# Kernel tuning notes

Measured on AMD Instinct MI355X. Metric: run time of the kernel, lower is better.

Reference implementation:

```python
import jax, jax.numpy as jnp
import numpy as np

N, E, IN, HID, OUT, H, G = 50000, 800000, 128, 32, 32, 4, 64
NEG_SLOPE = 0.2


def setup_inputs() -> dict:
    key = jax.random.key(0)
    ks = jax.random.split(key, 12)
    p = lambda k, s: jax.random.normal(k, s, jnp.float32) * 0.1
    x = jax.random.normal(ks[0], (N, IN), jnp.float32)
    edge_index = jax.random.randint(ks[1], (2, E), 0, N, dtype=jnp.int64)
    batch = jnp.sort(jax.random.randint(ks[2], (N,), 0, G, dtype=jnp.int64))
    return {
        'x': x, 'edge_index': edge_index, 'batch': batch,
        'W1': p(ks[3], (IN, H * HID)),
        'att_src1': p(ks[4], (H, HID)), 'att_dst1': p(ks[5], (H, HID)),
        'b1': jnp.zeros((H * HID,), jnp.float32),
        'W2': p(ks[6], (H * HID, H * OUT)),
        'att_src2': p(ks[7], (H, OUT)), 'att_dst2': p(ks[8], (H, OUT)),
        'b2': jnp.zeros((H * OUT,), jnp.float32),
        'lin_w': p(ks[9], (H * OUT, 1)),
        'lin_b': jnp.zeros((1,), jnp.float32),
    }


def gat_conv(x, src, dst, W, a_src, a_dst, b, heads, ch):
    # x: [N, F_in]; src/dst: [E'] with self-loops already appended.
    n = x.shape[0]
    h = (x @ W).reshape(n, heads, ch)                      # [N, H, C]
    alpha_s = jnp.einsum('nhc,hc->nh', h, a_src)           # [N, H]
    alpha_d = jnp.einsum('nhc,hc->nh', h, a_dst)
    e = jax.nn.leaky_relu(alpha_s[src] + alpha_d[dst], NEG_SLOPE)  # [E', H]
    # segment softmax over destination neighborhoods
    m = jax.ops.segment_max(e, dst, num_segments=n)
    m = jnp.where(jnp.isfinite(m), m, 0.0)
    ex = jnp.exp(e - m[dst])
    s = jax.ops.segment_sum(ex, dst, num_segments=n)
    alpha = ex / (s[dst] + 1e-16)                          # [E', H]
    out = jax.ops.segment_sum(alpha[:, :, None] * h[src], dst, num_segments=n)
    return out.reshape(n, heads * ch) + b


def reference(x, edge_index, batch, W1, att_src1, att_dst1, b1,
              W2, att_src2, att_dst2, b2, lin_w, lin_b):
    # add self-loops (PyG GATConv default add_self_loops=True)
    loops = jnp.arange(N, dtype=edge_index.dtype)
    src = jnp.concatenate([edge_index[0], loops])
    dst = jnp.concatenate([edge_index[1], loops])

    h = jax.nn.elu(gat_conv(x, src, dst, W1, att_src1, att_dst1, b1, H, HID))
    h = gat_conv(h, src, dst, W2, att_src2, att_dst2, b2, H, OUT)  # [N, H*OUT]

    # global mean + max pool per graph
    counts = jax.ops.segment_sum(jnp.ones((N,), h.dtype), batch, num_segments=G)
    mean_p = jax.ops.segment_sum(h, batch, num_segments=G) / jnp.maximum(counts, 1.0)[:, None]
    max_p = jax.ops.segment_max(h, batch, num_segments=G)
    max_p = jnp.where(jnp.isfinite(max_p), max_p, 0.0)
    pooled = mean_p + max_p                                # [G, H*OUT]
    return pooled @ lin_w + lin_b                          # [G, 1]
```

## Files before the change

### kernel.cpp

```cpp
#include <hip/hip_runtime.h>
#include <hip/hip_bf16.h>
#include <hip/hip_fp16.h>
#include <math.h>

#define NEG_SLOPE 0.2f
#define BCAP 80
#define LAYER_W 16384

typedef _Float16 half8 __attribute__((ext_vector_type(8)));
typedef _Float16 half4v __attribute__((ext_vector_type(4)));
typedef float f32x4 __attribute__((ext_vector_type(4)));


__device__ __forceinline__ int lbound(const int* __restrict__ a, int n, int key) {
    int lo = 0, hi = n;
    while (lo < hi) {
        int mid = (lo + hi) >> 1;
        if (a[mid] < key) lo = mid + 1; else hi = mid;
    }
    return lo;
}

__device__ __forceinline__ unsigned encf(float f) {
    unsigned u = __float_as_uint(f);
    return (u & 0x80000000u) ? ~u : (u | 0x80000000u);
}
__device__ __forceinline__ float decf(unsigned u) {
    return (u & 0x80000000u) ? __uint_as_float(u & 0x7FFFFFFFu) : __uint_as_float(~u);
}


__global__ void init_kernel(int* __restrict__ cnt, int* __restrict__ col,
                            float* __restrict__ gsum, unsigned* __restrict__ gmax,
                            int n, int gtot) {
    int i = blockIdx.x * blockDim.x + threadIdx.x;
    if (i < n) {
        cnt[i] = 1;
        col[(size_t)i * BCAP] = i;
    }
    if (i < gtot) { gsum[i] = 0.f; gmax[i] = 0x007FFFFFu;  }
}

__global__ void build_kernel(const int* __restrict__ src, const int* __restrict__ dst,
                             int* __restrict__ cnt, int* __restrict__ col, int E) {
    int i = blockIdx.x * blockDim.x + threadIdx.x;
    if (i >= E) return;
    int d = dst[i];
    int slot = atomicAdd(&cnt[d], 1);
    if (slot < BCAP) col[(size_t)d * BCAP + slot] = src[i];
}


__global__ void wprep_kernel(const float* __restrict__ W1, const float* __restrict__ W2,
                             _Float16* __restrict__ wt_hi, _Float16* __restrict__ wt_lo) {
    int b = blockIdx.x;
    int layer = b >> 5;
    int nt = (b >> 2) & 7;
    int kc = b & 3;
    const float* W = layer ? W2 : W1;
    int lane = threadIdx.x;
    int n = lane & 15, q = lane >> 4;
    size_t base = (size_t)layer * LAYER_W + (size_t)((nt * 4 + kc) * 64 + lane) * 8;
    #pragma unroll
    for (int j = 0; j < 8; ++j) {
        int k = kc * 32 + q * 8 + j;
        float w = W[(size_t)k * 128 + nt * 16 + n];
        _Float16 hi = (_Float16)w;
        wt_hi[base + j] = hi;
        wt_lo[base + j] = (_Float16)(w - (float)hi);
    }
}


__global__ __launch_bounds__(256) void gemm_attn_kernel(
        const float* __restrict__ A,
        const _Float16* __restrict__ wt_hi, const _Float16* __restrict__ wt_lo,
        const float* __restrict__ att_src, const float* __restrict__ att_dst,
        _Float16* __restrict__ H16, float* __restrict__ as_, float* __restrict__ ad_,
        int M) {
    __shared__ _Float16 a_hi[64][136];
    __shared__ _Float16 a_lo[64][136];

    int tid = threadIdx.x;
    int m0 = blockIdx.x * 64;

    #pragma unroll
    for (int t = 0; t < 8; ++t) {
        int f = tid + t * 256;
        int r = f >> 5;
        int c4 = (f & 31) << 2;
        int gr = m0 + r; if (gr >= M) gr = M - 1;
        const float4 v = *(const float4*)(A + (size_t)gr * 128 + c4);
        _Float16 h0 = (_Float16)v.x, h1 = (_Float16)v.y;
        _Float16 h2 = (_Float16)v.z, h3 = (_Float16)v.w;
        half4v hi = { h0, h1, h2, h3 };
        half4v lo = { (_Float16)(v.x - (float)h0), (_Float16)(v.y - (float)h1),
                      (_Float16)(v.z - (float)h2), (_Float16)(v.w - (float)h3) };
        *(half4v*)&a_hi[r][c4] = hi;
        *(half4v*)&a_lo[r][c4] = lo;
    }
    __syncthreads();

    int w = tid >> 6;
    int lane = tid & 63;
    int cbase = lane & 15;
    int q = lane >> 4;
    int mrow = (w << 4) + cbase;

    f32x4 acc[8];
    #pragma unroll
    for (int nt = 0; nt < 8; ++nt) acc[nt] = (f32x4){0.f, 0.f, 0.f, 0.f};

    #pragma unroll
    for (int kc = 0; kc < 4; ++kc) {
        half8 ah = *(half8*)&a_hi[mrow][kc * 32 + q * 8];
        half8 al = *(half8*)&a_lo[mrow][kc * 32 + q * 8];
        #pragma unroll
        for (int nt = 0; nt < 8; ++nt) {
            const half8 bh = *(const half8*)(wt_hi + (size_t)((nt * 4 + kc) * 64 + lane) * 8);
            const half8 bl = *(const half8*)(wt_lo + (size_t)((nt * 4 + kc) * 64 + lane) * 8);
            acc[nt] = __builtin_amdgcn_mfma_f32_16x16x32_f16(ah, bh, acc[nt], 0, 0, 0);
            acc[nt] = __builtin_amdgcn_mfma_f32_16x16x32_f16(al, bh, acc[nt], 0, 0, 0);
            acc[nt] = __builtin_amdgcn_mfma_f32_16x16x32_f16(ah, bl, acc[nt], 0, 0, 0);
        }
    }

    float ps[4][4], pd[4][4];
    #pragma unroll
    for (int h = 0; h < 4; ++h)
        #pragma unroll
        for (int i = 0; i < 4; ++i) { ps[h][i] = 0.f; pd[h][i] = 0.f; }

    #pragma unroll
    for (int nt = 0; nt < 8; ++nt) {
        int c = nt * 16 + cbase;
        float sv = att_src[c], dv = att_dst[c];
        int h = nt >> 1;
        #pragma unroll
        for (int i = 0; i < 4; ++i) {
            ps[h][i] += acc[nt][i] * sv;
            pd[h][i] += acc[nt][i] * dv;
            int gr = m0 + (w << 4) + (q << 2) + i;
            if (gr < M) H16[(size_t)gr * 128 + c] = (_Float16)acc[nt][i];
        }
    }
    #pragma unroll
    for (int h = 0; h < 4; ++h)
        #pragma unroll
        for (int i = 0; i < 4; ++i) {
            float a = ps[h][i], b = pd[h][i];
            #pragma unroll
            for (int off = 1; off < 16; off <<= 1) {
                a += __shfl_xor(a, off, 64);
                b += __shfl_xor(b, off, 64);
            }
            if (cbase == 0) {
                int gr = m0 + (w << 4) + (q << 2) + i;
                if (gr < M) { as_[(size_t)gr * 4 + h] = a; ad_[(size_t)gr * 4 + h] = b; }
            }
        }
}


__global__ __launch_bounds__(256) void agg_kernel(
        const int* __restrict__ cnt, const int* __restrict__ col,
        const _Float16* __restrict__ h16, const float* __restrict__ as_,
        const float* __restrict__ ad_, const float* __restrict__ bias,
        float* __restrict__ out, int n, int elu) {
    __shared__ int   s_col[4][64];
    __shared__ float s_w[4][256];
    __shared__ int   s_nchunk;

    int wvb  = threadIdx.x >> 6;
    int lane = threadIdx.x & 63;
    int wv   = blockIdx.x * 4 + wvb;
    int valid = (wv < n);
    if (!valid) wv = n - 1;

    int deg = cnt[wv]; if (deg > BCAP) deg = BCAP;
    const int* crow = col + (size_t)wv * BCAP;
    const float4 adv = *(const float4*)(ad_ + (size_t)wv * 4);

    if (threadIdx.x == 0) s_nchunk = 0;
    __syncthreads();
    if (lane == 0) atomicMax(&s_nchunk, (deg + 63) >> 6);
    __syncthreads();
    int nchunk = s_nchunk;

    int q = lane >> 4;
    int r = lane & 15;
    int head = r >> 2;
    const _Float16* hrow = h16 + 8 * r;

    float l0 = 0.f, l1 = 0.f, l2 = 0.f, l3 = 0.f;
    float acc[8];
    #pragma unroll
    for (int j = 0; j < 8; ++j) acc[j] = 0.f;

    for (int c = 0; c < nchunk; ++c) {
        int c0 = c << 6;
        int cl = deg - c0;
        cl = cl < 0 ? 0 : (cl > 64 ? 64 : cl);
        if (lane < cl) {
            int s = crow[c0 + lane];
            const float4 av = *(const float4*)(as_ + (size_t)s * 4);
            float e0 = av.x + adv.x, e1 = av.y + adv.y;
            float e2 = av.z + adv.z, e3 = av.w + adv.w;
            float w0 = __expf(fmaxf(e0, NEG_SLOPE * e0));
            float w1 = __expf(fmaxf(e1, NEG_SLOPE * e1));
            float w2 = __expf(fmaxf(e2, NEG_SLOPE * e2));
            float w3 = __expf(fmaxf(e3, NEG_SLOPE * e3));
            l0 += w0; l1 += w1; l2 += w2; l3 += w3;
            s_col[wvb][lane] = s;
            *(float4*)&s_w[wvb][lane * 4] = make_float4(w0, w1, w2, w3);
        } else {
            s_col[wvb][lane] = 0;
            *(float4*)&s_w[wvb][lane * 4] = make_float4(0.f, 0.f, 0.f, 0.f);
        }
        __syncthreads();
        for (int it = 0; it < cl; it += 16) {
            int ea = it + q;
            int eb = ea + 4;
            int ec = ea + 8;
            int ed = ea + 12;
            int sa = s_col[wvb][ea];
            int sb = s_col[wvb][eb];
            int sc = s_col[wvb][ec];
            int sd = s_col[wvb][ed];
            float wa = s_w[wvb][ea * 4 + head];
            float wb = s_w[wvb][eb * 4 + head];
            float wc = s_w[wvb][ec * 4 + head];
            float wd = s_w[wvb][ed * 4 + head];
            const half8 ha = *(const half8*)(hrow + (size_t)sa * 128);
            const half8 hb = *(const half8*)(hrow + (size_t)sb * 128);
            const half8 hc = *(const half8*)(hrow + (size_t)sc * 128);
            const half8 hd = *(const half8*)(hrow + (size_t)sd * 128);
            #pragma unroll
            for (int j = 0; j < 8; ++j)
                acc[j] += wa * (float)ha[j] + wb * (float)hb[j]
                        + wc * (float)hc[j] + wd * (float)hd[j];
        }
        __syncthreads();
    }

    #pragma unroll
    for (int j = 0; j < 8; ++j) {
        acc[j] += __shfl_xor(acc[j], 16, 64);
        acc[j] += __shfl_xor(acc[j], 32, 64);
    }

    #pragma unroll
    for (int off = 1; off < 64; off <<= 1) {
        l0 += __shfl_xor(l0, off, 64);
        l1 += __shfl_xor(l1, off, 64);
        l2 += __shfl_xor(l2, off, 64);
        l3 += __shfl_xor(l3, off, 64);
    }

    if (lane < 16 && valid) {
        float lh = head == 0 ? l0 : head == 1 ? l1 : head == 2 ? l2 : l3;
        float inv = 1.f / (lh + 1e-16f);
        const float4 bv0 = *(const float4*)(bias + 8 * r);
        const float4 bv1 = *(const float4*)(bias + 8 * r + 4);
        float o[8];
        o[0] = acc[0] * inv + bv0.x; o[1] = acc[1] * inv + bv0.y;
        o[2] = acc[2] * inv + bv0.z; o[3] = acc[3] * inv + bv0.w;
        o[4] = acc[4] * inv + bv1.x; o[5] = acc[5] * inv + bv1.y;
        o[6] = acc[6] * inv + bv1.z; o[7] = acc[7] * inv + bv1.w;
        if (elu) {
            #pragma unroll
            for (int j = 0; j < 8; ++j) o[j] = o[j] > 0.f ? o[j] : expm1f(o[j]);
        }
        *(float4*)(out + (size_t)wv * 128 + 8 * r)     = make_float4(o[0], o[1], o[2], o[3]);
        *(float4*)(out + (size_t)wv * 128 + 8 * r + 4) = make_float4(o[4], o[5], o[6], o[7]);
    }
}


__global__ void pool1_kernel(const float* __restrict__ h, const int* __restrict__ batch,
                             float* __restrict__ gsum, unsigned* __restrict__ gmax, int n) {
    int g = blockIdx.x >> 3;
    int p = blockIdx.x & 7;
    int c = threadIdx.x;
    int s = lbound(batch, n, g);
    int e = lbound(batch, n, g + 1);
    int len = e - s;
    int lo = s + (int)((long long)len * p / 8);
    int hi = s + (int)((long long)len * (p + 1) / 8);
    float sum = 0.f, mx = -INFINITY;
    for (int i = lo; i < hi; ++i) {
        float v = h[(size_t)i * 128 + c];
        sum += v; mx = fmaxf(mx, v);
    }
    if (hi > lo) {
        atomicAdd(&gsum[g * 128 + c], sum);
        atomicMax(&gmax[g * 128 + c], encf(mx));
    }
}

__global__ void pool2_kernel(const float* __restrict__ gsum, const unsigned* __restrict__ gmax,
                             const int* __restrict__ batch, const float* __restrict__ lin_w,
                             const float* __restrict__ lin_b, float* __restrict__ out, int n) {
    int g = blockIdx.x;
    int c = threadIdx.x;
    int s = lbound(batch, n, g);
    int e = lbound(batch, n, g + 1);
    float cnt = fmaxf((float)(e - s), 1.0f);
    float mean = gsum[g * 128 + c] / cnt;
    float mx = decf(gmax[g * 128 + c]);
    if (!isfinite(mx)) mx = 0.f;
    float v = (mean + mx) * lin_w[c];
    __shared__ float red[128];
    red[c] = v;
    __syncthreads();
    for (int off = 64; off > 0; off >>= 1) {
        if (c < off) red[c] += red[c + off];
        __syncthreads();
    }
    if (c == 0) out[g] = red[0] + lin_b[0];
}


extern "C" void kernel_launch(void* const* d_in, const int* in_sizes, int n_in,
                              void* d_out, int out_size, void* d_ws, size_t ws_size,
                              hipStream_t stream) {
    const float* x    = (const float*)d_in[0];
    const int*   ei   = (const int*)d_in[1];
    const int*   batch= (const int*)d_in[2];
    const float* W1   = (const float*)d_in[3];
    const float* at_s1= (const float*)d_in[4];
    const float* at_d1= (const float*)d_in[5];
    const float* b1   = (const float*)d_in[6];
    const float* W2   = (const float*)d_in[7];
    const float* at_s2= (const float*)d_in[8];
    const float* at_d2= (const float*)d_in[9];
    const float* b2   = (const float*)d_in[10];
    const float* lw   = (const float*)d_in[11];
    const float* lb   = (const float*)d_in[12];
    float* out = (float*)d_out;

    const int N = in_sizes[0] / 128;
    const int E = in_sizes[1] / 2;
    const int G = out_size;

    char* p = (char*)d_ws;
    auto carve = [&](size_t bytes) -> void* {
        void* q = (void*)p;
        p += (bytes + 255) & ~(size_t)255;
        return q;
    };
    _Float16* h16    = (_Float16*)carve((size_t)N * 128 * 2);
    float*    agg    = (float*)carve((size_t)N * 128 * 4);
    float*    asb    = (float*)carve((size_t)N * 4 * 4);
    float*    adb    = (float*)carve((size_t)N * 4 * 4);
    int*      cnt    = (int*)carve((size_t)N * 4);
    int*      col    = (int*)carve((size_t)N * BCAP * 4);
    float*    gsum   = (float*)carve((size_t)G * 128 * 4);
    unsigned* gmax   = (unsigned*)carve((size_t)G * 128 * 4);
    _Float16* wt_hi  = (_Float16*)carve((size_t)2 * LAYER_W * 2);
    _Float16* wt_lo  = (_Float16*)carve((size_t)2 * LAYER_W * 2);

    const int* esrc = ei;
    const int* edst = ei + E;

    int initN = (N > G * 128) ? N : G * 128;
    init_kernel<<<(initN + 255) / 256, 256, 0, stream>>>(cnt, col, gsum, gmax, N, G * 128);
    build_kernel<<<(E + 255) / 256, 256, 0, stream>>>(esrc, edst, cnt, col, E);
    wprep_kernel<<<64, 64, 0, stream>>>(W1, W2, wt_hi, wt_lo);

    gemm_attn_kernel<<<(N + 63) / 64, 256, 0, stream>>>(
        x, wt_hi, wt_lo, at_s1, at_d1, h16, asb, adb, N);
    agg_kernel<<<(N + 3) / 4, 256, 0, stream>>>(cnt, col, h16, asb, adb, b1, agg, N, 1);

    gemm_attn_kernel<<<(N + 63) / 64, 256, 0, stream>>>(
        agg, wt_hi + LAYER_W, wt_lo + LAYER_W, at_s2, at_d2, h16, asb, adb, N);
    agg_kernel<<<(N + 3) / 4, 256, 0, stream>>>(cnt, col, h16, asb, adb, b2, agg, N, 0);

    pool1_kernel<<<G * 8, 128, 0, stream>>>(agg, batch, gsum, gmax, N);
    pool2_kernel<<<G, 128, 0, stream>>>(gsum, gmax, batch, lw, lb, out, N);
}
```

Before: 311.9 us.

## Fold attention vectors into weights as extra GEMM tile; sum softmax denominators during aggregation

```diff
diff --git a/kernel.cpp b/kernel.cpp
--- a/kernel.cpp
+++ b/kernel.cpp
@@ -5,7 +5,7 @@
 
 #define NEG_SLOPE 0.2f
 #define BCAP 80
-#define LAYER_W 16384
+#define LAYER_W 18432
 
 typedef _Float16 half8 __attribute__((ext_vector_type(8)));
 typedef _Float16 half4v __attribute__((ext_vector_type(4)));
@@ -52,19 +52,32 @@
 
 
 __global__ void wprep_kernel(const float* __restrict__ W1, const float* __restrict__ W2,
+                             const float* __restrict__ as1, const float* __restrict__ ad1,
+                             const float* __restrict__ as2, const float* __restrict__ ad2,
                              _Float16* __restrict__ wt_hi, _Float16* __restrict__ wt_lo) {
     int b = blockIdx.x;
-    int layer = b >> 5;
-    int nt = (b >> 2) & 7;
-    int kc = b & 3;
-    const float* W = layer ? W2 : W1;
+    int layer = b / 36;
+    int rem = b % 36;
+    int nt = rem >> 2;
+    int kc = rem & 3;
+    const float* W  = layer ? W2 : W1;
+    const float* As = layer ? as2 : as1;
+    const float* Ad = layer ? ad2 : ad1;
     int lane = threadIdx.x;
     int n = lane & 15, q = lane >> 4;
     size_t base = (size_t)layer * LAYER_W + (size_t)((nt * 4 + kc) * 64 + lane) * 8;
     #pragma unroll
     for (int j = 0; j < 8; ++j) {
         int k = kc * 32 + q * 8 + j;
-        float w = W[(size_t)k * 128 + nt * 16 + n];
+        float w = 0.f;
+        if (nt < 8) {
+            w = W[(size_t)k * 128 + nt * 16 + n];
+        } else if (n < 4) {
+            for (int c = 0; c < 32; ++c) w += W[(size_t)k * 128 + n * 32 + c] * As[n * 32 + c];
+        } else if (n < 8) {
+            int hh = n - 4;
+            for (int c = 0; c < 32; ++c) w += W[(size_t)k * 128 + hh * 32 + c] * Ad[hh * 32 + c];
+        }
         _Float16 hi = (_Float16)w;
         wt_hi[base + j] = hi;
         wt_lo[base + j] = (_Float16)(w - (float)hi);
@@ -75,7 +88,6 @@
 __global__ __launch_bounds__(256) void gemm_attn_kernel(
         const float* __restrict__ A,
         const _Float16* __restrict__ wt_hi, const _Float16* __restrict__ wt_lo,
-        const float* __restrict__ att_src, const float* __restrict__ att_dst,
         _Float16* __restrict__ H16, float* __restrict__ as_, float* __restrict__ ad_,
         int M) {
     __shared__ _Float16 a_hi[64][136];
@@ -107,16 +119,16 @@
     int q = lane >> 4;
     int mrow = (w << 4) + cbase;
 
-    f32x4 acc[8];
-    #pragma unroll
-    for (int nt = 0; nt < 8; ++nt) acc[nt] = (f32x4){0.f, 0.f, 0.f, 0.f};
+    f32x4 acc[9];
+    #pragma unroll
+    for (int nt = 0; nt < 9; ++nt) acc[nt] = (f32x4){0.f, 0.f, 0.f, 0.f};
 
     #pragma unroll
     for (int kc = 0; kc < 4; ++kc) {
         half8 ah = *(half8*)&a_hi[mrow][kc * 32 + q * 8];
         half8 al = *(half8*)&a_lo[mrow][kc * 32 + q * 8];
         #pragma unroll
-        for (int nt = 0; nt < 8; ++nt) {
+        for (int nt = 0; nt < 9; ++nt) {
             const half8 bh = *(const half8*)(wt_hi + (size_t)((nt * 4 + kc) * 64 + lane) * 8);
             const half8 bl = *(const half8*)(wt_lo + (size_t)((nt * 4 + kc) * 64 + lane) * 8);
             acc[nt] = __builtin_amdgcn_mfma_f32_16x16x32_f16(ah, bh, acc[nt], 0, 0, 0);
@@ -125,40 +137,25 @@
         }
     }
 
-    float ps[4][4], pd[4][4];
-    #pragma unroll
-    for (int h = 0; h < 4; ++h)
-        #pragma unroll
-        for (int i = 0; i < 4; ++i) { ps[h][i] = 0.f; pd[h][i] = 0.f; }
-
     #pragma unroll
     for (int nt = 0; nt < 8; ++nt) {
         int c = nt * 16 + cbase;
-        float sv = att_src[c], dv = att_dst[c];
-        int h = nt >> 1;
         #pragma unroll
         for (int i = 0; i < 4; ++i) {
-            ps[h][i] += acc[nt][i] * sv;
-            pd[h][i] += acc[nt][i] * dv;
             int gr = m0 + (w << 4) + (q << 2) + i;
             if (gr < M) H16[(size_t)gr * 128 + c] = (_Float16)acc[nt][i];
         }
     }
-    #pragma unroll
-    for (int h = 0; h < 4; ++h)
+    if (cbase < 8) {
         #pragma unroll
         for (int i = 0; i < 4; ++i) {
-            float a = ps[h][i], b = pd[h][i];
-            #pragma unroll
-            for (int off = 1; off < 16; off <<= 1) {
-                a += __shfl_xor(a, off, 64);
-                b += __shfl_xor(b, off, 64);
+            int gr = m0 + (w << 4) + (q << 2) + i;
+            if (gr < M) {
+                if (cbase < 4) as_[(size_t)gr * 4 + cbase]     = acc[8][i];
+                else           ad_[(size_t)gr * 4 + cbase - 4] = acc[8][i];
             }
-            if (cbase == 0) {
-                int gr = m0 + (w << 4) + (q << 2) + i;
-                if (gr < M) { as_[(size_t)gr * 4 + h] = a; ad_[(size_t)gr * 4 + h] = b; }
-            }
-        }
+        }
+    }
 }
 
 
@@ -192,7 +189,7 @@
     int head = r >> 2;
     const _Float16* hrow = h16 + 8 * r;
 
-    float l0 = 0.f, l1 = 0.f, l2 = 0.f, l3 = 0.f;
+    float lsum = 0.f;
     float acc[8];
     #pragma unroll
     for (int j = 0; j < 8; ++j) acc[j] = 0.f;
@@ -210,7 +207,6 @@
             float w1 = __expf(fmaxf(e1, NEG_SLOPE * e1));
             float w2 = __expf(fmaxf(e2, NEG_SLOPE * e2));
             float w3 = __expf(fmaxf(e3, NEG_SLOPE * e3));
-            l0 += w0; l1 += w1; l2 += w2; l3 += w3;
             s_col[wvb][lane] = s;
             *(float4*)&s_w[wvb][lane * 4] = make_float4(w0, w1, w2, w3);
         } else {
@@ -235,6 +231,7 @@
             const half8 hb = *(const half8*)(hrow + (size_t)sb * 128);
             const half8 hc = *(const half8*)(hrow + (size_t)sc * 128);
             const half8 hd = *(const half8*)(hrow + (size_t)sd * 128);
+            lsum += wa + wb + wc + wd;
             #pragma unroll
             for (int j = 0; j < 8; ++j)
                 acc[j] += wa * (float)ha[j] + wb * (float)hb[j]
@@ -248,18 +245,11 @@
         acc[j] += __shfl_xor(acc[j], 16, 64);
         acc[j] += __shfl_xor(acc[j], 32, 64);
     }
-
-    #pragma unroll
-    for (int off = 1; off < 64; off <<= 1) {
-        l0 += __shfl_xor(l0, off, 64);
-        l1 += __shfl_xor(l1, off, 64);
-        l2 += __shfl_xor(l2, off, 64);
-        l3 += __shfl_xor(l3, off, 64);
-    }
+    lsum += __shfl_xor(lsum, 16, 64);
+    lsum += __shfl_xor(lsum, 32, 64);
 
     if (lane < 16 && valid) {
-        float lh = head == 0 ? l0 : head == 1 ? l1 : head == 2 ? l2 : l3;
-        float inv = 1.f / (lh + 1e-16f);
+        float inv = 1.f / (lsum + 1e-16f);
         const float4 bv0 = *(const float4*)(bias + 8 * r);
         const float4 bv1 = *(const float4*)(bias + 8 * r + 4);
         float o[8];
@@ -366,14 +356,14 @@
     int initN = (N > G * 128) ? N : G * 128;
     init_kernel<<<(initN + 255) / 256, 256, 0, stream>>>(cnt, col, gsum, gmax, N, G * 128);
     build_kernel<<<(E + 255) / 256, 256, 0, stream>>>(esrc, edst, cnt, col, E);
-    wprep_kernel<<<64, 64, 0, stream>>>(W1, W2, wt_hi, wt_lo);
+    wprep_kernel<<<72, 64, 0, stream>>>(W1, W2, at_s1, at_d1, at_s2, at_d2, wt_hi, wt_lo);
 
     gemm_attn_kernel<<<(N + 63) / 64, 256, 0, stream>>>(
-        x, wt_hi, wt_lo, at_s1, at_d1, h16, asb, adb, N);
+        x, wt_hi, wt_lo, h16, asb, adb, N);
     agg_kernel<<<(N + 3) / 4, 256, 0, stream>>>(cnt, col, h16, asb, adb, b1, agg, N, 1);
 
     gemm_attn_kernel<<<(N + 63) / 64, 256, 0, stream>>>(
-        agg, wt_hi + LAYER_W, wt_lo + LAYER_W, at_s2, at_d2, h16, asb, adb, N);
+        agg, wt_hi + LAYER_W, wt_lo + LAYER_W, h16, asb, adb, N);
     agg_kernel<<<(N + 3) / 4, 256, 0, stream>>>(cnt, col, h16, asb, adb, b2, agg, N, 0);
 
     pool1_kernel<<<G * 8, 128, 0, stream>>>(agg, batch, gsum, gmax, N);
```

Measured after the change: 305.4 us. 1.02x faster.
